# Optimization experiments

Measured on AMD Instinct MI355X. Metric: run time of the kernel, lower is better.

Reference implementation:

```python
import jax, jax.numpy as jnp
import numpy as np

B, S, D = 512, 200, 512
NQ, NC, NQD, NCD = 10000, 500, 101, 101


def _linear_params(key, fin, fout):
    # torch nn.Linear default init: U(-1/sqrt(fin), 1/sqrt(fin)); store W as (in,out)
    k1, k2 = jax.random.split(key)
    bound = 1.0 / np.sqrt(fin)
    W = jax.random.uniform(k1, (fin, fout), minval=-bound, maxval=bound, dtype=jnp.float32)
    b = jax.random.uniform(k2, (fout,), minval=-bound, maxval=bound, dtype=jnp.float32)
    return W, b


def setup_inputs() -> dict:
    key = jax.random.key(0)
    ks = jax.random.split(key, 16)
    inp = {
        'question_seq': jax.random.randint(ks[0], (B, S), 0, NQ),
        'concept_seq': jax.random.randint(ks[1], (B, S), 0, NC),
        'question_diff_seq': jax.random.randint(ks[2], (B, S), 0, NQD),
        'concept_diff_seq': jax.random.randint(ks[3], (B, S), 0, NCD),
        'correct_seq': jax.random.randint(ks[4], (B, S), 0, 2),
        'E_q': jax.random.normal(ks[5], (NQ, D), dtype=jnp.float32),
        'E_c': jax.random.normal(ks[6], (NC, D), dtype=jnp.float32),
        'E_qd': jax.random.normal(ks[7], (NQD, D), dtype=jnp.float32),
        'E_cd': jax.random.normal(ks[8], (NCD, D), dtype=jnp.float32),
        'E_corr': jax.random.normal(ks[9], (2, D), dtype=jnp.float32),
    }
    inp['W_x'], inp['b_x'] = _linear_params(ks[10], 4 * D, D)
    inp['W_s1'], inp['b_s1'] = _linear_params(ks[11], D, D)
    inp['W_s2'], inp['b_s2'] = _linear_params(ks[12], D, D)
    inp['W_p1'], inp['b_p1'] = _linear_params(ks[13], 2 * D, D)
    inp['W_p2'], inp['b_p2'] = _linear_params(ks[14], 2 * D, D)
    inp['W_ki'], inp['b_ki'] = _linear_params(ks[15], 4 * D, D)
    # h_pre: xavier_uniform on a (B, D) tensor -> U(-a, a), a = sqrt(6/(B+D))
    a = np.sqrt(6.0 / (B + D))
    inp['h0'] = jax.random.uniform(jax.random.key(1), (B, D), minval=-a, maxval=a, dtype=jnp.float32)
    return inp


def reference(question_seq, concept_seq, question_diff_seq, concept_diff_seq, correct_seq,
              E_q, E_c, E_qd, E_cd, E_corr,
              W_x, b_x, W_s1, b_s1, W_s2, b_s2, W_p1, b_p1, W_p2, b_p2, W_ki, b_ki, h0):
    # embedding lookups: [B, S, D]
    qe = E_q[question_seq]
    ce = E_c[concept_seq]
    qde = E_qd[question_diff_seq]
    cde = E_cd[concept_diff_seq]
    corr = E_corr[correct_seq]

    # generate_x_MLP applied to concat of 4 embeddings, vectorized over all t: [B, S, D]
    x_all = jnp.concatenate([qe, ce, qde, cde], axis=-1) @ W_x + b_x

    # time-major slices for scan over t = 0 .. S-2
    def tm(a):  # [B, S, D] -> [S, B, D]
        return jnp.swapaxes(a, 0, 1)

    xs = (tm(x_all)[:-1], tm(x_all)[1:], tm(corr)[:-1], tm(qde)[:-1], tm(cde)[:-1])

    def step(h_pre, t_in):
        x_t, x_next, ce_t, qd_t, cd_t = t_in
        d = x_t - h_pre
        # dropout in eval mode = identity
        sdf = jax.nn.sigmoid(d @ W_s1 + b_s1) * jnp.tanh(d @ W_s2 + b_s2)
        pka_in = jnp.concatenate([sdf, ce_t], axis=-1)
        pka = jax.nn.sigmoid(pka_in @ W_p1 + b_p1) * jnp.tanh(pka_in @ W_p2 + b_p2)
        ki_in = jnp.concatenate([h_pre, ce_t, qd_t, cd_t], axis=-1)
        gamma = jax.nn.sigmoid(ki_in @ W_ki + b_ki)
        h = gamma * h_pre + (1.0 - gamma) * pka
        y_t = jax.nn.sigmoid(jnp.sum(x_next * h, axis=-1))  # [B]
        return h, y_t

    _, y_seq = jax.lax.scan(step, h0, xs)  # y_seq: [S-1, B]
    y = jnp.concatenate([y_seq.T, jnp.zeros((question_seq.shape[0], 1), dtype=y_seq.dtype)], axis=1)
    return y  # [B, S], last column 0 as in the torch code
```

## Files before the change

kernel.cpp:

```cpp
#include <hip/hip_runtime.h>


typedef unsigned short u16;
using f32x4 = __attribute__((ext_vector_type(4))) float;
using bf16x8 = __attribute__((ext_vector_type(8))) short;

#define DEV static __device__ __forceinline__

#define Bv 512
#define Sv 200

DEV u16 f2bf(float f) {
  unsigned int u = __float_as_uint(f);
  unsigned int r = (u + 0x7fffu + ((u >> 16) & 1u)) >> 16;
  return (u16)r;
}
DEV float bf2f(u16 h) { return __uint_as_float(((unsigned int)h) << 16); }
DEV float sigm(float x) { return 1.0f / (1.0f + __expf(-x)); }
DEV float tanh_(float x) {
  x = fmaxf(fminf(x, 15.f), -15.f);
  float e = __expf(2.0f * x);
  return (e - 1.0f) / (e + 1.0f);
}
DEV f32x4 MF(bf16x8 a, bf16x8 b, f32x4 c) {
  return __builtin_amdgcn_mfma_f32_16x16x32_bf16(a, b, c, 0, 0, 0);
}

union LDU { f32x4 f; bf16x8 b; };
DEV void ld16v(f32x4* d, const u16* p) {
  asm volatile("global_load_dwordx4 %0, %1, off sc1" : "=v"(*d) : "v"(p));
}
DEV void st2v(u16* p, u16 v) {
  unsigned w = v;
  asm volatile("global_store_short %0, %1, off sc1" : : "v"(p), "v"(w) : "memory");
}
DEV void waitv0() {
  asm volatile("s_waitcnt vmcnt(0)" ::: "memory");
  __builtin_amdgcn_sched_barrier(0);
}

template <int NB, bool AF32>
DEV void gemm_tiles(const void* __restrict__ Aptr, int mvalid,
                    const u16* __restrict__ BT0, const u16* __restrict__ BT1,
                    u16* ldsA, u16* ldsB0, u16* ldsB1, int tid,
                    f32x4* acc0, f32x4* acc1) {
  const int lane = tid & 63, wid = tid >> 6;
  const int fr = lane & 15, fq = lane >> 4;
  const int srow = tid >> 2, sseg = tid & 3;

  for (int kt = 0; kt < 16; ++kt) {
    const int k0 = kt * 32;
    {
      bf16x8 pack;
      if constexpr (AF32) {
        if (srow < mvalid) {
          const float4* ap = (const float4*)((const float*)Aptr + (size_t)srow * 512 + k0 + sseg * 8);
          float4 v0 = ap[0], v1 = ap[1];
          pack[0] = (short)f2bf(v0.x); pack[1] = (short)f2bf(v0.y);
          pack[2] = (short)f2bf(v0.z); pack[3] = (short)f2bf(v0.w);
          pack[4] = (short)f2bf(v1.x); pack[5] = (short)f2bf(v1.y);
          pack[6] = (short)f2bf(v1.z); pack[7] = (short)f2bf(v1.w);
        } else {
          for (int j = 0; j < 8; ++j) pack[j] = 0;
        }
      } else {
        pack = *(const bf16x8*)((const u16*)Aptr + (size_t)srow * 512 + k0 + sseg * 8);
      }
      *(bf16x8*)&ldsA[srow * 40 + sseg * 8] = pack;
      *(bf16x8*)&ldsB0[srow * 40 + sseg * 8] =
          *(const bf16x8*)(BT0 + (size_t)srow * 512 + k0 + sseg * 8);
      if constexpr (NB == 2)
        *(bf16x8*)&ldsB1[srow * 40 + sseg * 8] =
            *(const bf16x8*)(BT1 + (size_t)srow * 512 + k0 + sseg * 8);
    }
    __syncthreads();
    bf16x8 a = *(const bf16x8*)&ldsA[(wid * 16 + fr) * 40 + fq * 8];
#pragma unroll
    for (int ni = 0; ni < 4; ++ni) {
      bf16x8 b0 = *(const bf16x8*)&ldsB0[(ni * 16 + fr) * 40 + fq * 8];
      acc0[ni] = MF(a, b0, acc0[ni]);
      if constexpr (NB == 2) {
        bf16x8 b1 = *(const bf16x8*)&ldsB1[(ni * 16 + fr) * 40 + fq * 8];
        acc1[ni] = MF(a, b1, acc1[ni]);
      }
    }
    __syncthreads();
  }
}

template <bool F32OUT>
__global__ __launch_bounds__(256) void gemm_table_k(const float* __restrict__ A, int M,
                                                    const u16* __restrict__ BT,
                                                    const float* __restrict__ bias,
                                                    void* __restrict__ C) {
  __shared__ u16 ldsA[64 * 40], ldsB[64 * 40];
  const int m0 = blockIdx.x * 64, n0 = blockIdx.y * 64;
  const int tid = threadIdx.x;
  f32x4 acc[4] = {};
  gemm_tiles<1, true>(A + (size_t)m0 * 512, M - m0, BT + (size_t)n0 * 512, nullptr,
                      ldsA, ldsB, nullptr, tid, acc, nullptr);
  const int lane = tid & 63, wid = tid >> 6, fr = lane & 15, fq = lane >> 4;
#pragma unroll
  for (int ni = 0; ni < 4; ++ni) {
    int col = n0 + ni * 16 + fr;
    float bv = bias ? bias[col] : 0.f;
#pragma unroll
    for (int r = 0; r < 4; ++r) {
      int row = m0 + wid * 16 + fq * 4 + r;
      if (row < M) {
        float v = acc[ni][r] + bv;
        if constexpr (F32OUT)
          ((float*)C)[(size_t)row * 512 + col] = v;
        else
          ((u16*)C)[(size_t)row * 512 + col] = f2bf(v);
      }
    }
  }
}

__global__ __launch_bounds__(256) void convT_k(const float* __restrict__ src, u16* __restrict__ dst) {
  __shared__ float tile[32][33];
  const int bi = blockIdx.x, bj = blockIdx.y;
  const int tx = threadIdx.x & 31, ty = threadIdx.x >> 5;
#pragma unroll
  for (int r = 0; r < 4; ++r)
    tile[ty + 8 * r][tx] = src[(size_t)(bj * 32 + ty + 8 * r) * 512 + bi * 32 + tx];
  __syncthreads();
#pragma unroll
  for (int r = 0; r < 4; ++r)
    dst[(size_t)(bi * 32 + ty + 8 * r) * 512 + bj * 32 + tx] = f2bf(tile[tx][ty + 8 * r]);
}

__global__ __launch_bounds__(256) void seqT_k(
    const int* __restrict__ q, const int* __restrict__ c, const int* __restrict__ qd,
    const int* __restrict__ cd, const int* __restrict__ corr,
    int* __restrict__ qT, int* __restrict__ cT, int* __restrict__ qdT,
    int* __restrict__ cdT, int* __restrict__ corrT) {
  const int i = blockIdx.x * 256 + threadIdx.x;
  const int b = i / Sv, t = i % Sv;
  const int o = t * Bv + b;
  qT[o] = q[i]; cT[o] = c[i]; qdT[o] = qd[i]; cdT[o] = cd[i]; corrT[o] = corr[i];
}

__global__ __launch_bounds__(256) void prologue_k(
    const float* __restrict__ h0, u16* __restrict__ hb, unsigned* __restrict__ flags) {
  const int i = blockIdx.x * 256 + threadIdx.x;
  if (i < 4096) flags[i] = 0u;
  hb[i] = f2bf(h0[i]);
}

DEV void load_wslice32(const u16* __restrict__ src, u16* dst, int n0, int tid) {
  for (int i = tid; i < 2048; i += 256) {
    int q = i & 3, kc = (i >> 2) & 15, c = i >> 6;
    int slot = c * 4 + (q ^ (c & 3) ^ ((c >> 2) & 3));
    *(bf16x8*)&dst[kc * 1024 + slot * 8] =
        *(const bf16x8*)&src[(size_t)(n0 + c) * 512 + kc * 32 + q * 8];
  }
}

DEV void mg_arrive(unsigned* myslot, unsigned phase, int tid) {
  waitv0();
  __syncthreads();
  __builtin_amdgcn_fence(__ATOMIC_RELEASE, "workgroup");
  if (tid == 0)
    __hip_atomic_store(myslot, phase, __ATOMIC_RELAXED, __HIP_MEMORY_SCOPE_AGENT);
}
DEV void mg_wait(unsigned* mgslots, unsigned phase, int tid) {
  if (tid < 16) {
    while (__hip_atomic_load(&mgslots[tid * 16], __ATOMIC_RELAXED,
                             __HIP_MEMORY_SCOPE_AGENT) < phase)
      __builtin_amdgcn_s_sleep(0);
  }
  __syncthreads();
  __builtin_amdgcn_fence(__ATOMIC_ACQUIRE, "workgroup");
}

__global__ __launch_bounds__(256, 1) void scan_k(
    const u16* __restrict__ Ws1T, const u16* __restrict__ Ws2T, const u16* __restrict__ WkihT,
    const u16* __restrict__ Wp1aT, const u16* __restrict__ Wp2aT,
    const u16* __restrict__ Kcorr, const u16* __restrict__ Kqd, const u16* __restrict__ Kcd,
    const u16* __restrict__ P1c, const u16* __restrict__ P2c,
    const u16* __restrict__ XQS1, const u16* __restrict__ XQS2,
    const u16* __restrict__ XCS1, const u16* __restrict__ XCS2,
    const u16* __restrict__ XQDS1, const u16* __restrict__ XQDS2,
    const u16* __restrict__ XCDS1, const u16* __restrict__ XCDS2,
    const int* __restrict__ qT, const int* __restrict__ cT, const int* __restrict__ qdT,
    const int* __restrict__ cdT, const int* __restrict__ corrT,
    const float* __restrict__ XQ, const float* __restrict__ XC, const float* __restrict__ XQD,
    const float* __restrict__ XCD, const float* __restrict__ h0,
    u16* __restrict__ sdf, u16* __restrict__ hb,
    float* __restrict__ dotpart, unsigned* __restrict__ flags) {
  __shared__ u16 wlds[32768];
  const int bid = blockIdx.x;
  const int mg = (bid & 7) | ((bid >> 7) << 3);
  const int ns = (bid >> 3) & 15;
  const int n0 = ns * 32;
  const int tid = threadIdx.x, lane = tid & 63, w = tid >> 6;
  const int rt = w >> 1, ct = w & 1;
  const int fr = lane & 15, fq = lane >> 4;

  load_wslice32(Ws1T, wlds,          n0, tid);
  load_wslice32(Ws2T, wlds + 16384,  n0, tid);

  const int col = n0 + ct * 16 + fr;
  const float kco0 = bf2f(Kcorr[col]), kco1 = bf2f(Kcorr[512 + col]);
  const float p1c0 = bf2f(P1c[col]),   p1c1 = bf2f(P1c[512 + col]);
  const float p2c0 = bf2f(P2c[col]),   p2c1 = bf2f(P2c[512 + col]);

  const int crow0 = mg * 32 + rt * 16 + fq * 4;
  const size_t aoff = (size_t)(mg * 32 + rt * 16 + fr) * 512 + fq * 8;
  const int slotr = (ct * 16 + fr) * 4 + (fq ^ (fr & 3) ^ ((fr >> 2) & 3));
  const u16* wb = wlds + slotr * 8;

  bf16x8 wkf[16], wp1f[16], wp2f[16];
#pragma unroll
  for (int kc = 0; kc < 16; ++kc) {
    wkf[kc]  = *(const bf16x8*)(WkihT + (size_t)col * 512 + kc * 32 + fq * 8);
    wp1f[kc] = *(const bf16x8*)(Wp1aT + (size_t)col * 512 + kc * 32 + fq * 8);
    wp2f[kc] = *(const bf16x8*)(Wp2aT + (size_t)col * 512 + kc * 32 + fq * 8);
  }

  unsigned* myslot  = flags + (mg * 16 + ns) * 16;
  unsigned* mgslots = flags + mg * 16 * 16;

  float hl[4];
#pragma unroll
  for (int r = 0; r < 4; ++r) hl[r] = h0[(size_t)(crow0 + r) * 512 + col];

  float xs1[4], xs2[4], kbias[4];
  int cis[4];
#pragma unroll
  for (int r = 0; r < 4; ++r) {
    const int row = crow0 + r;
    int qi = qT[row], cci = cT[row], qdi = qdT[row], cdi = cdT[row];
    int ci = corrT[row];
    xs1[r] = bf2f(XQS1[(size_t)qi * 512 + col]) + bf2f(XCS1[(size_t)cci * 512 + col]) +
             bf2f(XQDS1[(size_t)qdi * 512 + col]) + bf2f(XCDS1[(size_t)cdi * 512 + col]);
    xs2[r] = bf2f(XQS2[(size_t)qi * 512 + col]) + bf2f(XCS2[(size_t)cci * 512 + col]) +
             bf2f(XQDS2[(size_t)qdi * 512 + col]) + bf2f(XCDS2[(size_t)cdi * 512 + col]);
    cis[r] = ci;
    kbias[r] = (ci ? kco1 : kco0) + bf2f(Kqd[qdi * 512 + col]) + bf2f(Kcd[cdi * 512 + col]);
  }
  __syncthreads();

  for (int t = 0; t < Sv - 1; ++t) {
    LDU ah[16];
    __builtin_amdgcn_sched_barrier(0);
#pragma unroll
    for (int kc = 0; kc < 16; ++kc) ld16v(&ah[kc].f, hb + aoff + kc * 32);
    waitv0();
    f32x4 a1 = {}, a2 = {}, ag = {};
#pragma unroll
    for (int kc = 0; kc < 16; ++kc) {
      a1 = MF(ah[kc].b, *(const bf16x8*)(wb + kc * 1024), a1);
      a2 = MF(ah[kc].b, *(const bf16x8*)(wb + 16384 + kc * 1024), a2);
      ag = MF(ah[kc].b, wkf[kc], ag);
    }
    float g[4];
#pragma unroll
    for (int r = 0; r < 4; ++r) {
      g[r] = sigm(ag[r] + kbias[r]);
      float u1 = xs1[r] - a1[r];
      float u2 = xs2[r] - a2[r];
      st2v(&sdf[(size_t)(crow0 + r) * 512 + col], f2bf(sigm(u1) * tanh_(u2)));
    }
    mg_arrive(myslot, (unsigned)(2 * t + 1), tid);
    float xv[4];
#pragma unroll
    for (int r = 0; r < 4; ++r) {
      const int row = crow0 + r;
      int qi   = qT[(t + 1) * Bv + row];
      int cci  = cT[(t + 1) * Bv + row];
      int qdi2 = qdT[(t + 1) * Bv + row];
      int cdi2 = cdT[(t + 1) * Bv + row];
      xv[r] = XQ[(size_t)qi * 512 + col] + XC[(size_t)cci * 512 + col] +
              XQD[(size_t)qdi2 * 512 + col] + XCD[(size_t)cdi2 * 512 + col];
      xs1[r] = bf2f(XQS1[(size_t)qi * 512 + col]) + bf2f(XCS1[(size_t)cci * 512 + col]) +
               bf2f(XQDS1[(size_t)qdi2 * 512 + col]) + bf2f(XCDS1[(size_t)cdi2 * 512 + col]);
      xs2[r] = bf2f(XQS2[(size_t)qi * 512 + col]) + bf2f(XCS2[(size_t)cci * 512 + col]) +
               bf2f(XQDS2[(size_t)qdi2 * 512 + col]) + bf2f(XCDS2[(size_t)cdi2 * 512 + col]);
    }
    mg_wait(mgslots, (unsigned)(2 * t + 1), tid);

    LDU as[16];
    __builtin_amdgcn_sched_barrier(0);
#pragma unroll
    for (int kc = 0; kc < 16; ++kc) ld16v(&as[kc].f, sdf + aoff + kc * 32);
    waitv0();
    f32x4 ap1 = {}, ap2 = {};
#pragma unroll
    for (int kc = 0; kc < 16; ++kc) {
      ap1 = MF(as[kc].b, wp1f[kc], ap1);
      ap2 = MF(as[kc].b, wp2f[kc], ap2);
    }
    float dots[4];
#pragma unroll
    for (int r = 0; r < 4; ++r) {
      const int row = crow0 + r;
      float pka = sigm(ap1[r] + (cis[r] ? p1c1 : p1c0)) *
                  tanh_(ap2[r] + (cis[r] ? p2c1 : p2c0));
      float hn = g[r] * hl[r] + (1.f - g[r]) * pka;
      hl[r] = hn;
      st2v(&hb[(size_t)row * 512 + col], f2bf(hn));
      dots[r] = xv[r] * hn;
    }
    mg_arrive(myslot, (unsigned)(2 * t + 2), tid);
#pragma unroll
    for (int r = 0; r < 4; ++r) {
      float v = dots[r];
      v += __shfl_xor(v, 1);
      v += __shfl_xor(v, 2);
      v += __shfl_xor(v, 4);
      v += __shfl_xor(v, 8);
      if (fr == 0) dotpart[((size_t)t * Bv + crow0 + r) * 32 + ns * 2 + ct] = v;
    }
    if (t < Sv - 2) {
#pragma unroll
      for (int r = 0; r < 4; ++r) {
        const int row = crow0 + r;
        int ci = corrT[(t + 1) * Bv + row];
        int qdi = qdT[(t + 1) * Bv + row];
        int cdi = cdT[(t + 1) * Bv + row];
        cis[r] = ci;
        kbias[r] = (ci ? kco1 : kco0) + bf2f(Kqd[qdi * 512 + col]) +
                   bf2f(Kcd[cdi * 512 + col]);
      }
    }
    mg_wait(mgslots, (unsigned)(2 * t + 2), tid);
  }
}

__global__ __launch_bounds__(256) void finalize_k(const float* __restrict__ dotpart,
                                                  float* __restrict__ y) {
  const int i = blockIdx.x * 256 + threadIdx.x;
  const int b = i / Sv, t = i % Sv;
  float v = 0.f;
  if (t < Sv - 1) {
    const float4* p = (const float4*)&dotpart[((size_t)t * Bv + b) * 32];
    float s = 0.f;
#pragma unroll
    for (int k = 0; k < 8; ++k) {
      float4 q = p[k];
      s += q.x + q.y + q.z + q.w;
    }
    v = sigm(s);
  }
  y[i] = v;
}

extern "C" void kernel_launch(void* const* d_in, const int* in_sizes, int n_in,
                              void* d_out, int out_size, void* d_ws, size_t ws_size,
                              hipStream_t stream) {
  (void)in_sizes; (void)n_in; (void)out_size; (void)ws_size;
  const int* q_seq    = (const int*)d_in[0];
  const int* c_seq    = (const int*)d_in[1];
  const int* qd_seq   = (const int*)d_in[2];
  const int* cd_seq   = (const int*)d_in[3];
  const int* corr_seq = (const int*)d_in[4];
  const float* E_q    = (const float*)d_in[5];
  const float* E_c    = (const float*)d_in[6];
  const float* E_qd   = (const float*)d_in[7];
  const float* E_cd   = (const float*)d_in[8];
  const float* E_corr = (const float*)d_in[9];
  const float* W_x  = (const float*)d_in[10];
  const float* b_x  = (const float*)d_in[11];
  const float* W_s1 = (const float*)d_in[12];
  const float* b_s1 = (const float*)d_in[13];
  const float* W_s2 = (const float*)d_in[14];
  const float* b_s2 = (const float*)d_in[15];
  const float* W_p1 = (const float*)d_in[16];
  const float* b_p1 = (const float*)d_in[17];
  const float* W_p2 = (const float*)d_in[18];
  const float* b_p2 = (const float*)d_in[19];
  const float* W_ki = (const float*)d_in[20];
  const float* b_ki = (const float*)d_in[21];
  const float* h0   = (const float*)d_in[22];
  float* y = (float*)d_out;

  char* ws = (char*)d_ws;
  size_t off = 0;
  auto alloc = [&](size_t bytes) -> void* {
    void* p = ws + off;
    off += (bytes + 255) & ~(size_t)255;
    return p;
  };
  const size_t WSZ = 512 * 512 * sizeof(u16);
  u16* WxTq  = (u16*)alloc(WSZ);
  u16* WxTc  = (u16*)alloc(WSZ);
  u16* WxTqd = (u16*)alloc(WSZ);
  u16* WxTcd = (u16*)alloc(WSZ);
  u16* Ws1T  = (u16*)alloc(WSZ);
  u16* Ws2T  = (u16*)alloc(WSZ);
  u16* WkihT = (u16*)alloc(WSZ);
  u16* WkiTco = (u16*)alloc(WSZ);
  u16* WkiTqd = (u16*)alloc(WSZ);
  u16* WkiTcd = (u16*)alloc(WSZ);
  u16* Wp1aT = (u16*)alloc(WSZ);
  u16* Wp1hT = (u16*)alloc(WSZ);
  u16* Wp2aT = (u16*)alloc(WSZ);
  u16* Wp2hT = (u16*)alloc(WSZ);
  float* XQf  = (float*)alloc((size_t)10000 * 512 * 4);
  float* XCf  = (float*)alloc((size_t)500 * 512 * 4);
  float* XQDf = (float*)alloc((size_t)101 * 512 * 4);
  float* XCDf = (float*)alloc((size_t)101 * 512 * 4);
  u16* XQS1  = (u16*)alloc((size_t)10000 * 512 * 2);
  u16* XQS2  = (u16*)alloc((size_t)10000 * 512 * 2);
  u16* XCS1  = (u16*)alloc((size_t)500 * 512 * 2);
  u16* XCS2  = (u16*)alloc((size_t)500 * 512 * 2);
  u16* XQDS1 = (u16*)alloc((size_t)101 * 512 * 2);
  u16* XQDS2 = (u16*)alloc((size_t)101 * 512 * 2);
  u16* XCDS1 = (u16*)alloc((size_t)101 * 512 * 2);
  u16* XCDS2 = (u16*)alloc((size_t)101 * 512 * 2);
  u16* Kcorr = (u16*)alloc((size_t)2 * 512 * 2);
  u16* Kqd   = (u16*)alloc((size_t)101 * 512 * 2);
  u16* Kcd   = (u16*)alloc((size_t)101 * 512 * 2);
  u16* P1c   = (u16*)alloc((size_t)2 * 512 * 2);
  u16* P2c   = (u16*)alloc((size_t)2 * 512 * 2);
  u16* sdf   = (u16*)alloc((size_t)512 * 512 * 2);
  u16* hb    = (u16*)alloc((size_t)512 * 512 * 2);
  float* dotpart = (float*)alloc((size_t)199 * 512 * 32 * 4);
  int* qT    = (int*)alloc((size_t)Sv * Bv * 4);
  int* cT    = (int*)alloc((size_t)Sv * Bv * 4);
  int* qdT   = (int*)alloc((size_t)Sv * Bv * 4);
  int* cdT   = (int*)alloc((size_t)Sv * Bv * 4);
  int* corrT = (int*)alloc((size_t)Sv * Bv * 4);
  unsigned* flags = (unsigned*)alloc(8192 * 4);

  dim3 blk(256);
  dim3 tg(16, 16);
  convT_k<<<tg, blk, 0, stream>>>(W_x + 0 * 512 * 512, WxTq);
  convT_k<<<tg, blk, 0, stream>>>(W_x + 1 * 512 * 512, WxTc);
  convT_k<<<tg, blk, 0, stream>>>(W_x + 2 * 512 * 512, WxTqd);
  convT_k<<<tg, blk, 0, stream>>>(W_x + 3 * 512 * 512, WxTcd);
  convT_k<<<tg, blk, 0, stream>>>(W_s1, Ws1T);
  convT_k<<<tg, blk, 0, stream>>>(W_s2, Ws2T);
  convT_k<<<tg, blk, 0, stream>>>(W_ki + 0 * 512 * 512, WkihT);
  convT_k<<<tg, blk, 0, stream>>>(W_ki + 1 * 512 * 512, WkiTco);
  convT_k<<<tg, blk, 0, stream>>>(W_ki + 2 * 512 * 512, WkiTqd);
  convT_k<<<tg, blk, 0, stream>>>(W_ki + 3 * 512 * 512, WkiTcd);
  convT_k<<<tg, blk, 0, stream>>>(W_p1 + 0 * 512 * 512, Wp1aT);
  convT_k<<<tg, blk, 0, stream>>>(W_p1 + 1 * 512 * 512, Wp1hT);
  convT_k<<<tg, blk, 0, stream>>>(W_p2 + 0 * 512 * 512, Wp2aT);
  convT_k<<<tg, blk, 0, stream>>>(W_p2 + 1 * 512 * 512, Wp2hT);

  gemm_table_k<true><<<dim3(157, 8), blk, 0, stream>>>(E_q, 10000, WxTq, nullptr, XQf);
  gemm_table_k<true><<<dim3(8, 8), blk, 0, stream>>>(E_c, 500, WxTc, b_x, XCf);
  gemm_table_k<true><<<dim3(2, 8), blk, 0, stream>>>(E_qd, 101, WxTqd, nullptr, XQDf);
  gemm_table_k<true><<<dim3(2, 8), blk, 0, stream>>>(E_cd, 101, WxTcd, nullptr, XCDf);

  gemm_table_k<false><<<dim3(157, 8), blk, 0, stream>>>(XQf, 10000, Ws1T, nullptr, XQS1);
  gemm_table_k<false><<<dim3(157, 8), blk, 0, stream>>>(XQf, 10000, Ws2T, nullptr, XQS2);
  gemm_table_k<false><<<dim3(8, 8), blk, 0, stream>>>(XCf, 500, Ws1T, b_s1, XCS1);
  gemm_table_k<false><<<dim3(8, 8), blk, 0, stream>>>(XCf, 500, Ws2T, b_s2, XCS2);
  gemm_table_k<false><<<dim3(2, 8), blk, 0, stream>>>(XQDf, 101, Ws1T, nullptr, XQDS1);
  gemm_table_k<false><<<dim3(2, 8), blk, 0, stream>>>(XQDf, 101, Ws2T, nullptr, XQDS2);
  gemm_table_k<false><<<dim3(2, 8), blk, 0, stream>>>(XCDf, 101, Ws1T, nullptr, XCDS1);
  gemm_table_k<false><<<dim3(2, 8), blk, 0, stream>>>(XCDf, 101, Ws2T, nullptr, XCDS2);

  gemm_table_k<false><<<dim3(1, 8), blk, 0, stream>>>(E_corr, 2, WkiTco, b_ki, Kcorr);
  gemm_table_k<false><<<dim3(2, 8), blk, 0, stream>>>(E_qd, 101, WkiTqd, nullptr, Kqd);
  gemm_table_k<false><<<dim3(2, 8), blk, 0, stream>>>(E_cd, 101, WkiTcd, nullptr, Kcd);
  gemm_table_k<false><<<dim3(1, 8), blk, 0, stream>>>(E_corr, 2, Wp1hT, b_p1, P1c);
  gemm_table_k<false><<<dim3(1, 8), blk, 0, stream>>>(E_corr, 2, Wp2hT, b_p2, P2c);

  seqT_k<<<dim3(400), blk, 0, stream>>>(q_seq, c_seq, qd_seq, cd_seq, corr_seq,
                                        qT, cT, qdT, cdT, corrT);
  prologue_k<<<dim3(1024), blk, 0, stream>>>(h0, hb, flags);

  {
    const u16 *a0 = Ws1T, *a1 = Ws2T, *a2 = WkihT, *a3 = Wp1aT, *a4 = Wp2aT;
    const u16 *a5 = Kcorr, *a6 = Kqd, *a7 = Kcd, *a8 = P1c, *a9 = P2c;
    const u16 *a10 = XQS1, *a11 = XQS2, *a12 = XCS1, *a13 = XCS2;
    const u16 *a14 = XQDS1, *a15 = XQDS2, *a16 = XCDS1, *a17 = XCDS2;
    const int *a18 = qT, *a19 = cT, *a20 = qdT, *a21 = cdT, *a22 = corrT;
    const float *a23 = XQf, *a24 = XCf, *a25 = XQDf, *a26 = XCDf, *a27 = h0;
    u16 *a28 = sdf, *a29 = hb;
    float* a30 = dotpart;
    unsigned* a31 = flags;
    void* args[] = {&a0, &a1, &a2, &a3, &a4, &a5, &a6, &a7, &a8, &a9,
                    &a10, &a11, &a12, &a13, &a14, &a15, &a16, &a17,
                    &a18, &a19, &a20, &a21, &a22, &a23, &a24, &a25, &a26, &a27,
                    &a28, &a29, &a30, &a31};
    hipError_t e = hipLaunchCooperativeKernel((void*)scan_k, dim3(256), dim3(256),
                                              args, 0, stream);
    if (e != hipSuccess) {
      scan_k<<<dim3(256), dim3(256), 0, stream>>>(Ws1T, Ws2T, WkihT, Wp1aT, Wp2aT,
                                                  Kcorr, Kqd, Kcd, P1c, P2c,
                                                  XQS1, XQS2, XCS1, XCS2,
                                                  XQDS1, XQDS2, XCDS1, XCDS2,
                                                  qT, cT, qdT, cdT, corrT,
                                                  XQf, XCf, XQDf, XCDf, h0,
                                                  sdf, hb, dotpart, flags);
    }
  }

  finalize_k<<<dim3(400), blk, 0, stream>>>(dotpart, y);
}
```

Measured before the change: 2.324 ms.

## Share activation panel via LDS in scan, batch transposes, fuse dual table GEMMs

Inside the recurrent scan kernel, each wave now loads only half of the shared activation panel (h or sdf) from global memory and stages it in a swizzled LDS buffer, so the two column-tile waves that need the same rows no longer both fetch it. This halves global traffic per step at the cost of an extra LDS round-trip and a block barrier. The host side also merges the fourteen weight-transpose launches into one batched launch, and pairs the S1/S2 table GEMMs so each shares one A-tile load. Launch overhead and redundant A reads in the precompute stage go down.

```diff
diff --git a/kernel.cpp b/kernel.cpp
--- a/kernel.cpp
+++ b/kernel.cpp
@@ -118,8 +118,43 @@
   }
 }
 
-__global__ __launch_bounds__(256) void convT_k(const float* __restrict__ src, u16* __restrict__ dst) {
+__global__ __launch_bounds__(256) void gemm_table2_k(const float* __restrict__ A, int M,
+                                                     const u16* __restrict__ BT0,
+                                                     const u16* __restrict__ BT1,
+                                                     const float* __restrict__ bias0,
+                                                     const float* __restrict__ bias1,
+                                                     u16* __restrict__ C0,
+                                                     u16* __restrict__ C1) {
+  __shared__ u16 ldsA[64 * 40], ldsB0[64 * 40], ldsB1[64 * 40];
+  const int m0 = blockIdx.x * 64, n0 = blockIdx.y * 64;
+  const int tid = threadIdx.x;
+  f32x4 acc0[4] = {}, acc1[4] = {};
+  gemm_tiles<2, true>(A + (size_t)m0 * 512, M - m0, BT0 + (size_t)n0 * 512,
+                      BT1 + (size_t)n0 * 512, ldsA, ldsB0, ldsB1, tid, acc0, acc1);
+  const int lane = tid & 63, wid = tid >> 6, fr = lane & 15, fq = lane >> 4;
+#pragma unroll
+  for (int ni = 0; ni < 4; ++ni) {
+    int col = n0 + ni * 16 + fr;
+    float b0 = bias0 ? bias0[col] : 0.f;
+    float b1 = bias1 ? bias1[col] : 0.f;
+#pragma unroll
+    for (int r = 0; r < 4; ++r) {
+      int row = m0 + wid * 16 + fq * 4 + r;
+      if (row < M) {
+        C0[(size_t)row * 512 + col] = f2bf(acc0[ni][r] + b0);
+        C1[(size_t)row * 512 + col] = f2bf(acc1[ni][r] + b1);
+      }
+    }
+  }
+}
+
+struct CJ { const float* src; u16* dst; };
+struct CJobs { CJ j[14]; };
+__global__ __launch_bounds__(256) void convTB_k(CJobs jobs) {
   __shared__ float tile[32][33];
+  const int z = blockIdx.z;
+  const float* src = jobs.j[z].src;
+  u16* dst = jobs.j[z].dst;
   const int bi = blockIdx.x, bj = blockIdx.y;
   const int tx = threadIdx.x & 31, ty = threadIdx.x >> 5;
 #pragma unroll
@@ -191,6 +226,7 @@
     u16* __restrict__ sdf, u16* __restrict__ hb,
     float* __restrict__ dotpart, unsigned* __restrict__ flags) {
   __shared__ u16 wlds[32768];
+  __shared__ u16 panel[16384];
   const int bid = blockIdx.x;
   const int mg = (bid & 7) | ((bid >> 7) << 3);
   const int ns = (bid >> 3) & 15;
@@ -207,10 +243,12 @@
   const float p1c0 = bf2f(P1c[col]),   p1c1 = bf2f(P1c[512 + col]);
   const float p2c0 = bf2f(P2c[col]),   p2c1 = bf2f(P2c[512 + col]);
 
+  const int prow = rt * 16 + fr;
   const int crow0 = mg * 32 + rt * 16 + fq * 4;
-  const size_t aoff = (size_t)(mg * 32 + rt * 16 + fr) * 512 + fq * 8;
+  const size_t aoff = (size_t)(mg * 32 + prow) * 512;
   const int slotr = (ct * 16 + fr) * 4 + (fq ^ (fr & 3) ^ ((fr >> 2) & 3));
   const u16* wb = wlds + slotr * 8;
+  const int pslot = prow * 4 + (fq ^ (prow & 3) ^ ((prow >> 2) & 3));
 
   bf16x8 wkf[16], wp1f[16], wp2f[16];
 #pragma unroll
@@ -244,25 +282,36 @@
   __syncthreads();
 
   for (int t = 0; t < Sv - 1; ++t) {
-    LDU ah[16];
-    __builtin_amdgcn_sched_barrier(0);
-#pragma unroll
-    for (int kc = 0; kc < 16; ++kc) ld16v(&ah[kc].f, hb + aoff + kc * 32);
-    waitv0();
+    {
+      LDU tmp[8];
+      __builtin_amdgcn_sched_barrier(0);
+#pragma unroll
+      for (int j = 0; j < 8; ++j) {
+        const int kc = ct * 8 + j;
+        ld16v(&tmp[j].f, hb + aoff + kc * 32 + fq * 8);
+      }
+      waitv0();
+#pragma unroll
+      for (int j = 0; j < 8; ++j) {
+        const int kc = ct * 8 + j;
+        *(bf16x8*)&panel[kc * 1024 + pslot * 8] = tmp[j].b;
+      }
+    }
+    __syncthreads();
     f32x4 a1 = {}, a2 = {}, ag = {};
 #pragma unroll
     for (int kc = 0; kc < 16; ++kc) {
-      a1 = MF(ah[kc].b, *(const bf16x8*)(wb + kc * 1024), a1);
-      a2 = MF(ah[kc].b, *(const bf16x8*)(wb + 16384 + kc * 1024), a2);
-      ag = MF(ah[kc].b, wkf[kc], ag);
+      bf16x8 a = *(const bf16x8*)&panel[kc * 1024 + pslot * 8];
+      a1 = MF(a, *(const bf16x8*)(wb + kc * 1024), a1);
+      a2 = MF(a, *(const bf16x8*)(wb + 16384 + kc * 1024), a2);
+      ag = MF(a, wkf[kc], ag);
     }
     float g[4];
 #pragma unroll
     for (int r = 0; r < 4; ++r) {
       g[r] = sigm(ag[r] + kbias[r]);
-      float u1 = xs1[r] - a1[r];
-      float u2 = xs2[r] - a2[r];
-      st2v(&sdf[(size_t)(crow0 + r) * 512 + col], f2bf(sigm(u1) * tanh_(u2)));
+      st2v(&sdf[(size_t)(crow0 + r) * 512 + col],
+           f2bf(sigm(xs1[r] - a1[r]) * tanh_(xs2[r] - a2[r])));
     }
     mg_arrive(myslot, (unsigned)(2 * t + 1), tid);
     float xv[4];
@@ -282,16 +331,28 @@
     }
     mg_wait(mgslots, (unsigned)(2 * t + 1), tid);
 
-    LDU as[16];
-    __builtin_amdgcn_sched_barrier(0);
-#pragma unroll
-    for (int kc = 0; kc < 16; ++kc) ld16v(&as[kc].f, sdf + aoff + kc * 32);
-    waitv0();
+    {
+      LDU tmp[8];
+      __builtin_amdgcn_sched_barrier(0);
+#pragma unroll
+      for (int j = 0; j < 8; ++j) {
+        const int kc = ct * 8 + j;
+        ld16v(&tmp[j].f, sdf + aoff + kc * 32 + fq * 8);
+      }
+      waitv0();
+#pragma unroll
+      for (int j = 0; j < 8; ++j) {
+        const int kc = ct * 8 + j;
+        *(bf16x8*)&panel[kc * 1024 + pslot * 8] = tmp[j].b;
+      }
+    }
+    __syncthreads();
     f32x4 ap1 = {}, ap2 = {};
 #pragma unroll
     for (int kc = 0; kc < 16; ++kc) {
-      ap1 = MF(as[kc].b, wp1f[kc], ap1);
-      ap2 = MF(as[kc].b, wp2f[kc], ap2);
+      bf16x8 a = *(const bf16x8*)&panel[kc * 1024 + pslot * 8];
+      ap1 = MF(a, wp1f[kc], ap1);
+      ap2 = MF(a, wp2f[kc], ap2);
     }
     float dots[4];
 #pragma unroll
@@ -427,35 +488,31 @@
   unsigned* flags = (unsigned*)alloc(8192 * 4);
 
   dim3 blk(256);
-  dim3 tg(16, 16);
-  convT_k<<<tg, blk, 0, stream>>>(W_x + 0 * 512 * 512, WxTq);
-  convT_k<<<tg, blk, 0, stream>>>(W_x + 1 * 512 * 512, WxTc);
-  convT_k<<<tg, blk, 0, stream>>>(W_x + 2 * 512 * 512, WxTqd);
-  convT_k<<<tg, blk, 0, stream>>>(W_x + 3 * 512 * 512, WxTcd);
-  convT_k<<<tg, blk, 0, stream>>>(W_s1, Ws1T);
-  convT_k<<<tg, blk, 0, stream>>>(W_s2, Ws2T);
-  convT_k<<<tg, blk, 0, stream>>>(W_ki + 0 * 512 * 512, WkihT);
-  convT_k<<<tg, blk, 0, stream>>>(W_ki + 1 * 512 * 512, WkiTco);
-  convT_k<<<tg, blk, 0, stream>>>(W_ki + 2 * 512 * 512, WkiTqd);
-  convT_k<<<tg, blk, 0, stream>>>(W_ki + 3 * 512 * 512, WkiTcd);
-  convT_k<<<tg, blk, 0, stream>>>(W_p1 + 0 * 512 * 512, Wp1aT);
-  convT_k<<<tg, blk, 0, stream>>>(W_p1 + 1 * 512 * 512, Wp1hT);
-  convT_k<<<tg, blk, 0, stream>>>(W_p2 + 0 * 512 * 512, Wp2aT);
-  convT_k<<<tg, blk, 0, stream>>>(W_p2 + 1 * 512 * 512, Wp2hT);
+  {
+    CJobs jobs;
+    const float* srcs[14] = {W_x, W_x + 512 * 512, W_x + 2 * 512 * 512, W_x + 3 * 512 * 512,
+                             W_s1, W_s2, W_ki, W_ki + 512 * 512, W_ki + 2 * 512 * 512,
+                             W_ki + 3 * 512 * 512, W_p1, W_p1 + 512 * 512,
+                             W_p2, W_p2 + 512 * 512};
+    u16* dsts[14] = {WxTq, WxTc, WxTqd, WxTcd, Ws1T, Ws2T, WkihT, WkiTco, WkiTqd,
+                     WkiTcd, Wp1aT, Wp1hT, Wp2aT, Wp2hT};
+    for (int i = 0; i < 14; ++i) { jobs.j[i].src = srcs[i]; jobs.j[i].dst = dsts[i]; }
+    convTB_k<<<dim3(16, 16, 14), blk, 0, stream>>>(jobs);
+  }
 
   gemm_table_k<true><<<dim3(157, 8), blk, 0, stream>>>(E_q, 10000, WxTq, nullptr, XQf);
   gemm_table_k<true><<<dim3(8, 8), blk, 0, stream>>>(E_c, 500, WxTc, b_x, XCf);
   gemm_table_k<true><<<dim3(2, 8), blk, 0, stream>>>(E_qd, 101, WxTqd, nullptr, XQDf);
   gemm_table_k<true><<<dim3(2, 8), blk, 0, stream>>>(E_cd, 101, WxTcd, nullptr, XCDf);
 
-  gemm_table_k<false><<<dim3(157, 8), blk, 0, stream>>>(XQf, 10000, Ws1T, nullptr, XQS1);
-  gemm_table_k<false><<<dim3(157, 8), blk, 0, stream>>>(XQf, 10000, Ws2T, nullptr, XQS2);
-  gemm_table_k<false><<<dim3(8, 8), blk, 0, stream>>>(XCf, 500, Ws1T, b_s1, XCS1);
-  gemm_table_k<false><<<dim3(8, 8), blk, 0, stream>>>(XCf, 500, Ws2T, b_s2, XCS2);
-  gemm_table_k<false><<<dim3(2, 8), blk, 0, stream>>>(XQDf, 101, Ws1T, nullptr, XQDS1);
-  gemm_table_k<false><<<dim3(2, 8), blk, 0, stream>>>(XQDf, 101, Ws2T, nullptr, XQDS2);
-  gemm_table_k<false><<<dim3(2, 8), blk, 0, stream>>>(XCDf, 101, Ws1T, nullptr, XCDS1);
-  gemm_table_k<false><<<dim3(2, 8), blk, 0, stream>>>(XCDf, 101, Ws2T, nullptr, XCDS2);
+  gemm_table2_k<<<dim3(157, 8), blk, 0, stream>>>(XQf, 10000, Ws1T, Ws2T,
+                                                  nullptr, nullptr, XQS1, XQS2);
+  gemm_table2_k<<<dim3(8, 8), blk, 0, stream>>>(XCf, 500, Ws1T, Ws2T,
+                                                b_s1, b_s2, XCS1, XCS2);
+  gemm_table2_k<<<dim3(2, 8), blk, 0, stream>>>(XQDf, 101, Ws1T, Ws2T,
+                                                nullptr, nullptr, XQDS1, XQDS2);
+  gemm_table2_k<<<dim3(2, 8), blk, 0, stream>>>(XCDf, 101, Ws1T, Ws2T,
+                                                nullptr, nullptr, XCDS1, XCDS2);
 
   gemm_table_k<false><<<dim3(1, 8), blk, 0, stream>>>(E_corr, 2, WkiTco, b_ki, Kcorr);
   gemm_table_k<false><<<dim3(2, 8), blk, 0, stream>>>(E_qd, 101, WkiTqd, nullptr, Kqd);
```

Result: faster. 2.036 ms (-12.4%).
